# Performance work log

Measured on AMD Instinct MI355X. Metric: run time of the kernel, lower is better.

## Reference

```python
import jax, jax.numpy as jnp
import numpy as np

N_NODES = 100000
N_EDGES = 1600000
F_IN = 128
HID = 128
N_GRAPHS = 64


def setup_inputs() -> dict:
    key = jax.random.key(0)
    ks = jax.random.split(key, 8)
    x = jax.random.normal(ks[0], (N_NODES, F_IN), dtype=jnp.float32)
    edge_index = jax.random.randint(ks[1], (2, N_EDGES), 0, N_NODES, dtype=jnp.int64)
    batch = jnp.sort(jax.random.randint(ks[2], (N_NODES,), 0, N_GRAPHS, dtype=jnp.int64))
    s1 = 1.0 / np.sqrt(F_IN)
    s2 = 1.0 / np.sqrt(HID)
    W1 = jax.random.normal(ks[3], (F_IN, HID), dtype=jnp.float32) * s1
    b1 = jnp.zeros((HID,), dtype=jnp.float32)
    W2 = jax.random.normal(ks[4], (HID, HID), dtype=jnp.float32) * s2
    b2 = jnp.zeros((HID,), dtype=jnp.float32)
    fc_w = jax.random.normal(ks[5], (HID, 1), dtype=jnp.float32) * s2
    fc_b = jnp.zeros((1,), dtype=jnp.float32)
    return {"x": x, "edge_index": edge_index, "batch": batch,
            "W1": W1, "b1": b1, "W2": W2, "b2": b2, "fc_w": fc_w, "fc_b": fc_b}


def _gcn_norm(edge_index, num_nodes):
    # PyG GCNConv default: add self-loops, symmetric normalization.
    row = jnp.concatenate([edge_index[0], jnp.arange(num_nodes, dtype=edge_index.dtype)])
    col = jnp.concatenate([edge_index[1], jnp.arange(num_nodes, dtype=edge_index.dtype)])
    deg = jax.ops.segment_sum(jnp.ones_like(col, dtype=jnp.float32), col, num_segments=num_nodes)
    dinv = jnp.where(deg > 0, deg ** -0.5, 0.0)
    norm = dinv[row] * dinv[col]  # [E+N]
    return row, col, norm


def _gcn_conv(x, W, b, row, col, norm, num_nodes):
    xw = x @ W                                 # [N, H]
    msg = norm[:, None] * xw[row]              # gather along edges [E+N, H]
    out = jax.ops.segment_sum(msg, col, num_segments=num_nodes)  # scatter-add
    return out + b


def reference(x, edge_index, batch, W1, b1, W2, b2, fc_w, fc_b):
    num_nodes = x.shape[0]
    row, col, norm = _gcn_norm(edge_index, num_nodes)
    h = jax.nn.relu(_gcn_conv(x, W1, b1, row, col, norm, num_nodes))
    h = jax.nn.relu(_gcn_conv(h, W2, b2, row, col, norm, num_nodes))
    # global_mean_pool
    sums = jax.ops.segment_sum(h, batch, num_segments=N_GRAPHS)          # [G, H]
    cnts = jax.ops.segment_sum(jnp.ones((num_nodes,), jnp.float32), batch, num_segments=N_GRAPHS)
    pooled = sums / jnp.maximum(cnts, 1.0)[:, None]
    out = pooled @ fc_w + fc_b                 # [G, 1]
    return out.squeeze(-1)                     # [G]
```

## Files before the change

### kernel.cpp

```cpp
#include <hip/hip_runtime.h>
#include <hip/hip_bf16.h>
#include <math.h>


typedef __attribute__((ext_vector_type(8))) short bf16x8;
typedef __attribute__((ext_vector_type(4))) float f32x4;

union U4 { uint4 u; bf16x8 h; };

#define BKT_BITS 7
#define BKT_SZ 128
#define NB_MAX 1024
#define EPB 6400

__device__ inline unsigned pack_bf16(float a, float b) {
    __hip_bfloat16 ha = __float2bfloat16(a);
    __hip_bfloat16 hb = __float2bfloat16(b);
    unsigned short ua = *(unsigned short*)&ha;
    unsigned short ub = *(unsigned short*)&hb;
    return (unsigned)ua | ((unsigned)ub << 16);
}

__device__ inline float2 unpack_bf16(unsigned u) {
    return make_float2(__uint_as_float(u << 16), __uint_as_float(u & 0xffff0000u));
}

__global__ __launch_bounds__(256) void bucket_count_kernel(const int* __restrict__ col,
                                                           int* __restrict__ gcnt,
                                                           int E, int NB) {
    __shared__ int h[NB_MAX];
    for (int i = threadIdx.x; i < NB; i += 256) h[i] = 0;
    __syncthreads();
    int stride = gridDim.x * 256;
    for (int e = blockIdx.x * 256 + threadIdx.x; e < E; e += stride)
        atomicAdd(&h[col[e] >> BKT_BITS], 1);
    __syncthreads();
    for (int i = threadIdx.x; i < NB; i += 256) {
        int v = h[i];
        if (v) atomicAdd(&gcnt[i], v);
    }
}

__global__ void bucket_scan_kernel(const int* __restrict__ gcnt, int* __restrict__ ebase,
                                   int* __restrict__ cursor, int NB, int E) {
    __shared__ int sh[NB_MAX];
    int t = threadIdx.x;
    int orig = (t < NB) ? gcnt[t] : 0;
    sh[t] = orig; __syncthreads();
    for (int off = 1; off < NB_MAX; off <<= 1) {
        int v = (t >= off) ? sh[t - off] : 0;
        __syncthreads();
        sh[t] += v;
        __syncthreads();
    }
    if (t < NB) { int ex = sh[t] - orig; ebase[t] = ex; cursor[t] = ex; }
    if (t == 0) ebase[NB] = E;
}

__global__ __launch_bounds__(256) void bucket_scatter_kernel(const int* __restrict__ row,
                                                             const int* __restrict__ col,
                                                             int* __restrict__ cursor,
                                                             int2* __restrict__ binned,
                                                             int E) {
    __shared__ int2 eds[EPB];
    __shared__ int cnt[NB_MAX];
    __shared__ int base[NB_MAX];
    int e0 = blockIdx.x * EPB;
    int n = min(EPB, E - e0);
    for (int i = threadIdx.x; i < NB_MAX; i += 256) cnt[i] = 0;
    __syncthreads();
    for (int i = threadIdx.x; i < n; i += 256) {
        int c = col[e0 + i];
        eds[i] = make_int2(row[e0 + i], c);
        atomicAdd(&cnt[c >> BKT_BITS], 1);
    }
    __syncthreads();
    for (int i = threadIdx.x; i < NB_MAX; i += 256) {
        int k = cnt[i];
        base[i] = k ? atomicAdd(&cursor[i], k) : 0;
        cnt[i] = 0;
    }
    __syncthreads();
    for (int i = threadIdx.x; i < n; i += 256) {
        int2 ed = eds[i];
        int b = ed.y >> BKT_BITS;
        int rk = atomicAdd(&cnt[b], 1);
        binned[base[b] + rk] = make_int2(ed.x, ed.y & (BKT_SZ - 1));
    }
}

__global__ __launch_bounds__(256) void bucket_sort_kernel(const int2* __restrict__ binned,
                                                          const int* __restrict__ ebase,
                                                          int* __restrict__ rowptr,
                                                          float* __restrict__ dinv,
                                                          int* __restrict__ srcidx,
                                                          int N, int E) {
    int b = blockIdx.x;
    int v0 = b << BKT_BITS;
    int nn = min(BKT_SZ, N - v0);
    int s0 = ebase[b], s1 = ebase[b + 1];
    __shared__ int cnt[BKT_SZ];
    __shared__ int loc[BKT_SZ];
    __shared__ int cur[BKT_SZ];
    int t = threadIdx.x;
    if (t < BKT_SZ) cnt[t] = 0;
    __syncthreads();
    for (int i = s0 + t; i < s1; i += 256) atomicAdd(&cnt[binned[i].y], 1);
    __syncthreads();
    if (t < BKT_SZ) loc[t] = cnt[t];
    __syncthreads();
    for (int off = 1; off < BKT_SZ; off <<= 1) {
        int v = (t < BKT_SZ && t >= off) ? loc[t - off] : 0;
        __syncthreads();
        if (t < BKT_SZ) loc[t] += v;
        __syncthreads();
    }
    if (t < nn) {
        int ex = loc[t] - cnt[t];
        rowptr[v0 + t] = s0 + ex;
        cur[t] = ex;
        dinv[v0 + t] = rsqrtf((float)(cnt[t] + 1));
    }
    if (b == 0 && t == 0) rowptr[N] = E;
    __syncthreads();
    for (int i = s0 + t; i < s1; i += 256) {
        int2 ed = binned[i];
        int rk = atomicAdd(&cur[ed.y], 1);
        srcidx[s0 + rk] = ed.x;
    }
}

__global__ void bounds_kernel(const int* __restrict__ batch, int* __restrict__ start,
                              int N, int G) {
    int g = threadIdx.x;
    if (g > G) return;
    if (g == G) { start[G] = N; return; }
    int lo = 0, hi = N;
    while (lo < hi) { int mid = (lo + hi) >> 1; if (batch[mid] < g) lo = mid + 1; else hi = mid; }
    start[g] = lo;
}

__global__ void wprep_kernel(const float* __restrict__ W1, const float* __restrict__ W2,
                             unsigned* __restrict__ Wf1, unsigned* __restrict__ Wf2) {
    int bi = blockIdx.x, t = threadIdx.x;
    const float* W = (bi < 32) ? W1 : W2;
    unsigned* Wf = (bi < 32) ? Wf1 : Wf2;
    int f = bi & 31;
    int l = t >> 2, i = t & 3;
    int n = (f >> 2) * 16 + (l & 15);
    int k = (f & 3) * 32 + 8 * (l >> 4) + 2 * i;
    Wf[f * 256 + t] = pack_bf16(W[k * 128 + n], W[(k + 1) * 128 + n]);
}

template<bool IN_F32>
__global__ __launch_bounds__(256) void gemm_mfma(const void* __restrict__ Xv,
                                                 const unsigned* __restrict__ Wf,
                                                 const float* __restrict__ dinv,
                                                 unsigned* __restrict__ Yb, int N) {
    __shared__ unsigned wl[8192];
    for (int i = threadIdx.x; i < 2048; i += 256)
        ((uint4*)wl)[i] = ((const uint4*)Wf)[i];
    __syncthreads();

    const int w  = threadIdx.x >> 6;
    const int l  = threadIdx.x & 63;
    const int lm = l & 15;
    const int lg = l >> 4;
    const int base_row = blockIdx.x * 128 + w * 32;

    for (int t = 0; t < 2; ++t) {
        const int row = base_row + t * 16 + lm;
        const bool ok = row < N;
        U4 a[4];
        if (IN_F32) {
            const float* X = (const float*)Xv;
            #pragma unroll
            for (int kk = 0; kk < 4; ++kk) {
                if (ok) {
                    const float* p = X + (size_t)row * 128 + kk * 32 + lg * 8;
                    float4 q0 = *(const float4*)(p);
                    float4 q1 = *(const float4*)(p + 4);
                    a[kk].u = make_uint4(pack_bf16(q0.x, q0.y), pack_bf16(q0.z, q0.w),
                                         pack_bf16(q1.x, q1.y), pack_bf16(q1.z, q1.w));
                } else a[kk].u = make_uint4(0, 0, 0, 0);
            }
        } else {
            const uint4* X = (const uint4*)Xv;
            #pragma unroll
            for (int kk = 0; kk < 4; ++kk)
                a[kk].u = ok ? X[(size_t)row * 16 + kk * 4 + lg] : make_uint4(0, 0, 0, 0);
        }

        f32x4 acc[8];
        #pragma unroll
        for (int nt = 0; nt < 8; ++nt) acc[nt] = (f32x4){0.f, 0.f, 0.f, 0.f};

        #pragma unroll
        for (int kk = 0; kk < 4; ++kk) {
            #pragma unroll
            for (int nt = 0; nt < 8; ++nt) {
                bf16x8 b = *(const bf16x8*)&wl[(nt * 4 + kk) * 256 + l * 4];
                acc[nt] = __builtin_amdgcn_mfma_f32_16x16x32_bf16(a[kk].h, b, acc[nt], 0, 0, 0);
            }
        }

        #pragma unroll
        for (int r = 0; r < 4; ++r) {
            const int orow = base_row + t * 16 + lg * 4 + r;
            const float dv = (orow < N) ? dinv[orow] : 0.f;
            #pragma unroll
            for (int nt = 0; nt < 8; ++nt) {
                float v = acc[nt][r] * dv;
                float pv = __shfl_xor(v, 1, 64);
                if (!(lm & 1) && orow < N)
                    Yb[(size_t)orow * 64 + nt * 8 + (lm >> 1)] = pack_bf16(v, pv);
            }
        }
    }
}

__device__ inline void accum8(float* a, uint4 u) {
    float2 f0 = unpack_bf16(u.x), f1 = unpack_bf16(u.y);
    float2 f2 = unpack_bf16(u.z), f3 = unpack_bf16(u.w);
    a[0] += f0.x; a[1] += f0.y; a[2] += f1.x; a[3] += f1.y;
    a[4] += f2.x; a[5] += f2.y; a[6] += f3.x; a[7] += f3.y;
}

__device__ inline uint4 ldrow(const char* __restrict__ base, int s, unsigned flb) {
    return *(const uint4*)(base + ((unsigned)s * 256u + flb));
}

template<bool FC>
__global__ __launch_bounds__(256) void gather_kernel(const unsigned* __restrict__ xwb,
                                                     const float* __restrict__ dinv,
                                                     const float* __restrict__ b,
                                                     const int* __restrict__ rowptr,
                                                     const int* __restrict__ srcidx,
                                                     const float* __restrict__ fcw,
                                                     unsigned* __restrict__ outb,
                                                     float* __restrict__ outs, int N) {
    int wid = threadIdx.x >> 6, lane = threadIdx.x & 63;
    int v = blockIdx.x * 4 + wid;
    if (v >= N) return;
    int e0 = rowptr[v], e1 = rowptr[v + 1];
    int q = lane >> 4, fl = lane & 15;
    unsigned flb = (unsigned)fl * 16u;

    const char* base = (const char*)xwb;
    uint4 self = ldrow(base, v, flb);

    float a[8] = {0.f, 0.f, 0.f, 0.f, 0.f, 0.f, 0.f, 0.f};
    int e = e0 + q;
    for (; e + 12 < e1; e += 16) {
        int s0i = srcidx[e], s1i = srcidx[e + 4];
        int s2i = srcidx[e + 8], s3i = srcidx[e + 12];
        uint4 u0 = ldrow(base, s0i, flb);
        uint4 u1 = ldrow(base, s1i, flb);
        uint4 u2 = ldrow(base, s2i, flb);
        uint4 u3 = ldrow(base, s3i, flb);
        accum8(a, u0); accum8(a, u1); accum8(a, u2); accum8(a, u3);
    }
    if (e + 4 < e1) {
        int s0i = srcidx[e], s1i = srcidx[e + 4];
        uint4 u0 = ldrow(base, s0i, flb);
        uint4 u1 = ldrow(base, s1i, flb);
        accum8(a, u0); accum8(a, u1);
        e += 8;
    }
    if (e < e1) {
        accum8(a, ldrow(base, srcidx[e], flb));
    }

    #pragma unroll
    for (int j = 0; j < 8; ++j) {
        a[j] += __shfl_xor(a[j], 16, 64);
        a[j] += __shfl_xor(a[j], 32, 64);
    }

    float d = dinv[v];
    float2 s0 = unpack_bf16(self.x), s1 = unpack_bf16(self.y);
    float2 s2 = unpack_bf16(self.z), s3 = unpack_bf16(self.w);
    float4 bb0 = *(const float4*)(b + fl * 8);
    float4 bb1 = *(const float4*)(b + fl * 8 + 4);
    float h0 = fmaxf(fmaf(d, s0.x + a[0], bb0.x), 0.f);
    float h1 = fmaxf(fmaf(d, s0.y + a[1], bb0.y), 0.f);
    float h2 = fmaxf(fmaf(d, s1.x + a[2], bb0.z), 0.f);
    float h3 = fmaxf(fmaf(d, s1.y + a[3], bb0.w), 0.f);
    float h4 = fmaxf(fmaf(d, s2.x + a[4], bb1.x), 0.f);
    float h5 = fmaxf(fmaf(d, s2.y + a[5], bb1.y), 0.f);
    float h6 = fmaxf(fmaf(d, s3.x + a[6], bb1.z), 0.f);
    float h7 = fmaxf(fmaf(d, s3.y + a[7], bb1.w), 0.f);

    if (!FC) {
        if (q == 0) {
            uint4 p;
            p.x = pack_bf16(h0, h1); p.y = pack_bf16(h2, h3);
            p.z = pack_bf16(h4, h5); p.w = pack_bf16(h6, h7);
            *(uint4*)(outb + (size_t)v * 64 + fl * 4) = p;
        }
    } else {
        float4 w0 = *(const float4*)(fcw + fl * 8);
        float4 w1 = *(const float4*)(fcw + fl * 8 + 4);
        float s = h0 * w0.x + h1 * w0.y + h2 * w0.z + h3 * w0.w
                + h4 * w1.x + h5 * w1.y + h6 * w1.z + h7 * w1.w;
        #pragma unroll
        for (int m = 8; m > 0; m >>= 1) s += __shfl_xor(s, m, 64);
        if (lane == 0) outs[v] = s;
    }
}

__global__ __launch_bounds__(256) void pool_kernel(const float* __restrict__ s,
                                                   const int* __restrict__ start,
                                                   const float* __restrict__ fc_b,
                                                   float* __restrict__ out) {
    int g = blockIdx.x;
    int s0 = start[g], s1 = start[g + 1];
    float acc = 0.f;
    for (int v = s0 + threadIdx.x; v < s1; v += 256) acc += s[v];
    __shared__ float red[256];
    red[threadIdx.x] = acc;
    __syncthreads();
    #pragma unroll
    for (int off = 128; off > 0; off >>= 1) {
        if (threadIdx.x < off) red[threadIdx.x] += red[threadIdx.x + off];
        __syncthreads();
    }
    if (threadIdx.x == 0) {
        float cnt = (float)(s1 - s0);
        out[g] = red[0] / fmaxf(cnt, 1.f) + fc_b[0];
    }
}

extern "C" void kernel_launch(void* const* d_in, const int* in_sizes, int n_in,
                              void* d_out, int out_size, void* d_ws, size_t ws_size,
                              hipStream_t stream) {
    const float* x     = (const float*)d_in[0];
    const int*   ei    = (const int*)d_in[1];
    const int*   batch = (const int*)d_in[2];
    const float* W1    = (const float*)d_in[3];
    const float* b1    = (const float*)d_in[4];
    const float* W2    = (const float*)d_in[5];
    const float* b2    = (const float*)d_in[6];
    const float* fcw   = (const float*)d_in[7];
    const float* fcb   = (const float*)d_in[8];
    float* out = (float*)d_out;

    const int N = in_sizes[2];
    const int E = in_sizes[1] / 2;
    const int G = out_size;
    const int* row = ei;
    const int* col = ei + E;
    const int NB = (N + BKT_SZ - 1) >> BKT_BITS;

    auto align512 = [](size_t v) { return (v + 511) & ~(size_t)511; };
    char* ws = (char*)d_ws;
    size_t o = 0;
    int*      gcnt     = (int*)(ws + o);      o += align512((size_t)NB_MAX * 4);
    int*      ebase    = (int*)(ws + o);      o += align512((size_t)(NB_MAX + 1) * 4);
    int*      cursor   = (int*)(ws + o);      o += align512((size_t)NB_MAX * 4);
    float*    dinv     = (float*)(ws + o);    o += align512((size_t)N * 4);
    int*      rowptr   = (int*)(ws + o);      o += align512((size_t)(N + 1) * 4);
    int*      start    = (int*)(ws + o);      o += align512((size_t)(G + 1) * 4);
    float*    nodesc   = (float*)(ws + o);    o += align512((size_t)N * 4);
    unsigned* Wf1      = (unsigned*)(ws + o); o += align512(8192 * 4);
    unsigned* Wf2      = (unsigned*)(ws + o); o += align512(8192 * 4);
    int2*     binned   = (int2*)(ws + o);     o += align512((size_t)E * 8);
    int*      srcidx   = (int*)(ws + o);      o += align512((size_t)E * 4);
    unsigned* bufBF    = (unsigned*)(ws + o); o += align512((size_t)N * 64 * 4);
    unsigned* bufBF2   = (unsigned*)(ws + o);

    hipMemsetAsync(gcnt, 0, (size_t)NB * 4, stream);
    bucket_count_kernel<<<256, 256, 0, stream>>>(col, gcnt, E, NB);
    bucket_scan_kernel<<<1, NB_MAX, 0, stream>>>(gcnt, ebase, cursor, NB, E);
    bucket_scatter_kernel<<<(E + EPB - 1) / EPB, 256, 0, stream>>>(row, col, cursor, binned, E);
    bucket_sort_kernel<<<NB, 256, 0, stream>>>(binned, ebase, rowptr, dinv, srcidx, N, E);

    bounds_kernel<<<1, 128, 0, stream>>>(batch, start, N, G);
    wprep_kernel<<<64, 256, 0, stream>>>(W1, W2, Wf1, Wf2);

    const int gemm_blocks = (N + 127) / 128;
    const int gather_blocks = (N + 3) / 4;

    gemm_mfma<true><<<gemm_blocks, 256, 0, stream>>>(x, Wf1, dinv, bufBF, N);
    gather_kernel<false><<<gather_blocks, 256, 0, stream>>>(bufBF, dinv, b1, rowptr, srcidx,
                                                            nullptr, bufBF2, nullptr, N);

    gemm_mfma<false><<<gemm_blocks, 256, 0, stream>>>(bufBF2, Wf2, dinv, bufBF, N);
    gather_kernel<true><<<gather_blocks, 256, 0, stream>>>(bufBF, dinv, b2, rowptr, srcidx,
                                                           fcw, nullptr, nodesc, N);

    pool_kernel<<<G, 256, 0, stream>>>(nodesc, start, fcb, out);
}
```

Before: 235.0 us.

## Pack binned edges to 32-bit, fold bounds into scan, double GEMM rows per block

Binned edges are stored as one packed 32-bit word (source index shifted left, local destination in the low bits) instead of an int2, which halves the traffic of the scatter and sort passes. The scatter kernel drops its large shared-memory edge staging buffer and re-reads row and col from global memory instead. The graph-bounds binary search is folded into a second block of the scan kernel to save a launch. The GEMM now covers 256 rows per block, loading the weights into LDS half as often at the cost of fewer blocks. Packing assumes node indices fit in 25 bits, which holds for 100k nodes.

```diff
diff --git a/kernel.cpp b/kernel.cpp
--- a/kernel.cpp
+++ b/kernel.cpp
@@ -42,9 +42,19 @@
 }
 
 __global__ void bucket_scan_kernel(const int* __restrict__ gcnt, int* __restrict__ ebase,
-                                   int* __restrict__ cursor, int NB, int E) {
+                                   int* __restrict__ cursor, int NB, int E,
+                                   const int* __restrict__ batch, int* __restrict__ start,
+                                   int N, int G) {
+    int t = threadIdx.x;
+    if (blockIdx.x == 1) {
+        if (t > G) return;
+        if (t == G) { start[G] = N; return; }
+        int lo = 0, hi = N;
+        while (lo < hi) { int mid = (lo + hi) >> 1; if (batch[mid] < t) lo = mid + 1; else hi = mid; }
+        start[t] = lo;
+        return;
+    }
     __shared__ int sh[NB_MAX];
-    int t = threadIdx.x;
     int orig = (t < NB) ? gcnt[t] : 0;
     sh[t] = orig; __syncthreads();
     for (int off = 1; off < NB_MAX; off <<= 1) {
@@ -60,20 +70,16 @@
 __global__ __launch_bounds__(256) void bucket_scatter_kernel(const int* __restrict__ row,
                                                              const int* __restrict__ col,
                                                              int* __restrict__ cursor,
-                                                             int2* __restrict__ binned,
+                                                             unsigned* __restrict__ binned,
                                                              int E) {
-    __shared__ int2 eds[EPB];
     __shared__ int cnt[NB_MAX];
     __shared__ int base[NB_MAX];
     int e0 = blockIdx.x * EPB;
     int n = min(EPB, E - e0);
     for (int i = threadIdx.x; i < NB_MAX; i += 256) cnt[i] = 0;
     __syncthreads();
-    for (int i = threadIdx.x; i < n; i += 256) {
-        int c = col[e0 + i];
-        eds[i] = make_int2(row[e0 + i], c);
-        atomicAdd(&cnt[c >> BKT_BITS], 1);
-    }
+    for (int i = threadIdx.x; i < n; i += 256)
+        atomicAdd(&cnt[col[e0 + i] >> BKT_BITS], 1);
     __syncthreads();
     for (int i = threadIdx.x; i < NB_MAX; i += 256) {
         int k = cnt[i];
@@ -82,14 +88,14 @@
     }
     __syncthreads();
     for (int i = threadIdx.x; i < n; i += 256) {
-        int2 ed = eds[i];
-        int b = ed.y >> BKT_BITS;
+        int c = col[e0 + i];
+        int b = c >> BKT_BITS;
         int rk = atomicAdd(&cnt[b], 1);
-        binned[base[b] + rk] = make_int2(ed.x, ed.y & (BKT_SZ - 1));
-    }
-}
-
-__global__ __launch_bounds__(256) void bucket_sort_kernel(const int2* __restrict__ binned,
+        binned[base[b] + rk] = ((unsigned)row[e0 + i] << BKT_BITS) | (unsigned)(c & (BKT_SZ - 1));
+    }
+}
+
+__global__ __launch_bounds__(256) void bucket_sort_kernel(const unsigned* __restrict__ binned,
                                                           const int* __restrict__ ebase,
                                                           int* __restrict__ rowptr,
                                                           float* __restrict__ dinv,
@@ -105,7 +111,8 @@
     int t = threadIdx.x;
     if (t < BKT_SZ) cnt[t] = 0;
     __syncthreads();
-    for (int i = s0 + t; i < s1; i += 256) atomicAdd(&cnt[binned[i].y], 1);
+    for (int i = s0 + t; i < s1; i += 256)
+        atomicAdd(&cnt[binned[i] & (BKT_SZ - 1)], 1);
     __syncthreads();
     if (t < BKT_SZ) loc[t] = cnt[t];
     __syncthreads();
@@ -124,20 +131,10 @@
     if (b == 0 && t == 0) rowptr[N] = E;
     __syncthreads();
     for (int i = s0 + t; i < s1; i += 256) {
-        int2 ed = binned[i];
-        int rk = atomicAdd(&cur[ed.y], 1);
-        srcidx[s0 + rk] = ed.x;
-    }
-}
-
-__global__ void bounds_kernel(const int* __restrict__ batch, int* __restrict__ start,
-                              int N, int G) {
-    int g = threadIdx.x;
-    if (g > G) return;
-    if (g == G) { start[G] = N; return; }
-    int lo = 0, hi = N;
-    while (lo < hi) { int mid = (lo + hi) >> 1; if (batch[mid] < g) lo = mid + 1; else hi = mid; }
-    start[g] = lo;
+        unsigned ed = binned[i];
+        int rk = atomicAdd(&cur[ed & (BKT_SZ - 1)], 1);
+        srcidx[s0 + rk] = (int)(ed >> BKT_BITS);
+    }
 }
 
 __global__ void wprep_kernel(const float* __restrict__ W1, const float* __restrict__ W2,
@@ -166,9 +163,9 @@
     const int l  = threadIdx.x & 63;
     const int lm = l & 15;
     const int lg = l >> 4;
-    const int base_row = blockIdx.x * 128 + w * 32;
-
-    for (int t = 0; t < 2; ++t) {
+    const int base_row = blockIdx.x * 256 + w * 64;
+
+    for (int t = 0; t < 4; ++t) {
         const int row = base_row + t * 16 + lm;
         const bool ok = row < N;
         U4 a[4];
@@ -364,21 +361,21 @@
     float*    nodesc   = (float*)(ws + o);    o += align512((size_t)N * 4);
     unsigned* Wf1      = (unsigned*)(ws + o); o += align512(8192 * 4);
     unsigned* Wf2      = (unsigned*)(ws + o); o += align512(8192 * 4);
-    int2*     binned   = (int2*)(ws + o);     o += align512((size_t)E * 8);
+    unsigned* binned   = (unsigned*)(ws + o); o += align512((size_t)E * 4);
     int*      srcidx   = (int*)(ws + o);      o += align512((size_t)E * 4);
     unsigned* bufBF    = (unsigned*)(ws + o); o += align512((size_t)N * 64 * 4);
     unsigned* bufBF2   = (unsigned*)(ws + o);
 
     hipMemsetAsync(gcnt, 0, (size_t)NB * 4, stream);
     bucket_count_kernel<<<256, 256, 0, stream>>>(col, gcnt, E, NB);
-    bucket_scan_kernel<<<1, NB_MAX, 0, stream>>>(gcnt, ebase, cursor, NB, E);
+    bucket_scan_kernel<<<2, NB_MAX, 0, stream>>>(gcnt, ebase, cursor, NB, E,
+                                                 batch, start, N, G);
     bucket_scatter_kernel<<<(E + EPB - 1) / EPB, 256, 0, stream>>>(row, col, cursor, binned, E);
     bucket_sort_kernel<<<NB, 256, 0, stream>>>(binned, ebase, rowptr, dinv, srcidx, N, E);
 
-    bounds_kernel<<<1, 128, 0, stream>>>(batch, start, N, G);
     wprep_kernel<<<64, 256, 0, stream>>>(W1, W2, Wf1, Wf2);
 
-    const int gemm_blocks = (N + 127) / 128;
+    const int gemm_blocks = (N + 255) / 256;
     const int gather_blocks = (N + 3) / 4;
 
     gemm_mfma<true><<<gemm_blocks, 256, 0, stream>>>(x, Wf1, dinv, bufBF, N);
```

Result: no change. 234.9 us (-0.0%).
